# Kernel tuning notes

Hardware: AMD Instinct MI355X
Metric: run time of the kernel (lower is better)

## Reference

```python
import jax, jax.numpy as jnp
import numpy as np


def setup_inputs() -> dict:
    key = jax.random.key(0)
    k1, k2 = jax.random.split(key)
    x = jax.random.normal(k1, (8, 64, 256, 256), dtype=jnp.float32)
    gamma = jax.random.normal(k2, (1,), dtype=jnp.float32)
    return {"x": x, "gamma": gamma}


def reference(x, gamma):
    # NOTE: the torch code does `proj_query -= avg` in-place on a view of x,
    # so proj_value (another view of x) is ALSO mean-centered. We replicate that.
    B, C, H, W = x.shape
    n = H * W
    q = x.reshape(B, C, n)
    q = q - jnp.mean(q, axis=2, keepdims=True)  # centered channels, [B,C,N]
    # energy[b,c,d] = (1/n) * sum_n q[b,c,n]*q[b,d,n]  -> [B,C,C] covariance
    energy = jnp.einsum('bcn,bdn->bcd', q, q) / n
    attention = jax.nn.softmax(energy, axis=-1)
    out = jnp.einsum('bcd,bdn->bcn', attention, q).reshape(B, C, H, W)
    return gamma * out
```

## Files before the change

### kernel.cpp

```cpp
#include <hip/hip_runtime.h>
#include <hip/hip_bf16.h>

typedef __attribute__((ext_vector_type(8))) short short8;
typedef __attribute__((ext_vector_type(4))) short short4v;
typedef __attribute__((ext_vector_type(4))) float f32x4;
typedef __attribute__((ext_vector_type(8))) __bf16 bf16x8;

#define BB 8
#define CC 64
#define NN 65536
#define SPLIT1 64
#define COLS1 (NN / SPLIT1)
#define TILE_C 128
#define NT1 (COLS1 / TILE_C)
#define SPLIT3 128

__device__ inline short f2bf(float f) {
    __hip_bfloat16 h = __float2bfloat16(f);
    return __builtin_bit_cast(short, h);
}

template <typename V>
__device__ inline auto mfma_bf16_impl(V a, V b, f32x4 c, int)
    -> decltype(__builtin_amdgcn_mfma_f32_16x16x32_bf16(a, b, c, 0, 0, 0)) {
    return __builtin_amdgcn_mfma_f32_16x16x32_bf16(a, b, c, 0, 0, 0);
}
template <typename V>
__device__ inline f32x4 mfma_bf16_impl(V a, V b, f32x4 c, long) {
    bf16x8 a2 = __builtin_bit_cast(bf16x8, a);
    bf16x8 b2 = __builtin_bit_cast(bf16x8, b);
    return __builtin_amdgcn_mfma_f32_16x16x32_bf16(a2, b2, c, 0, 0, 0);
}
__device__ inline f32x4 mfma16(short8 a, short8 b, f32x4 c) {
    return mfma_bf16_impl(a, b, c, 0);
}

__device__ inline void stage_tile(const float* __restrict__ xb, int colbase,
                                  float* buf, int tid) {
    const int half = tid >> 5;
    const int sl   = tid & 31;
#pragma unroll
    for (int i = 0; i < 8; ++i) {
        const int row   = i * 8 + half;
        const int gbyte = (sl * 16) ^ ((row & 31) << 4);
        const float* gp = xb + (size_t)row * NN + colbase + (gbyte >> 2);
        float* lp = buf + i * 1024 + tid * 4;
#if __has_builtin(__builtin_amdgcn_global_load_lds)
        __builtin_amdgcn_global_load_lds(
            (const __attribute__((address_space(1))) void*)gp,
            (__attribute__((address_space(3))) void*)lp, 16, 0, 0);
#else
        *reinterpret_cast<f32x4*>(lp) = *reinterpret_cast<const f32x4*>(gp);
#endif
    }
}

__device__ inline void lds_read8(const float* buf, int row, int c0, float* v) {
    const char* rb = (const char*)(buf + row * TILE_C);
    const int swz = (row & 31) << 4;
    const f32x4 u0 = *reinterpret_cast<const f32x4*>(rb + ((c0 * 4) ^ swz));
    const f32x4 u1 = *reinterpret_cast<const f32x4*>(rb + (((c0 * 4) + 16) ^ swz));
    v[0] = u0[0]; v[1] = u0[1]; v[2] = u0[2]; v[3] = u0[3];
    v[4] = u1[0]; v[5] = u1[1]; v[6] = u1[2]; v[7] = u1[3];
}

__device__ inline short8 cvt8(const float* v) {
    short8 r;
#pragma unroll
    for (int j = 0; j < 8; ++j) r[j] = f2bf(v[j]);
    return r;
}

__global__ __launch_bounds__(256) void k1_gram(const float* __restrict__ x,
                                               float* __restrict__ partialG,
                                               float* __restrict__ partialS) {
    __shared__ float lbuf[2][CC * TILE_C];
    const int blk  = blockIdx.x;
    const int b    = blk / SPLIT1;
    const int s    = blk % SPLIT1;
    const int tid  = threadIdx.x;
    const int w    = tid >> 6, lane = tid & 63, lg = lane >> 4, lr = lane & 15;
    const float* xb = x + (size_t)b * CC * NN;
    const int colbase0 = s * COLS1;

    f32x4 acc[4];
#pragma unroll
    for (int dt = 0; dt < 4; ++dt) acc[dt] = (f32x4){0.f, 0.f, 0.f, 0.f};
    float asum = 0.f;

    stage_tile(xb, colbase0, lbuf[0], tid);
    __syncthreads();

    for (int t = 0; t < NT1; ++t) {
        if (t + 1 < NT1)
            stage_tile(xb, colbase0 + (t + 1) * TILE_C, lbuf[(t + 1) & 1], tid);
        const float* buf = lbuf[t & 1];
#pragma unroll
        for (int kk = 0; kk < TILE_C / 32; ++kk) {
            const int c0 = kk * 32 + lg * 8;
            float av[8];
            lds_read8(buf, w * 16 + lr, c0, av);
#pragma unroll
            for (int j = 0; j < 8; ++j) asum += av[j];
            const short8 af = cvt8(av);
#pragma unroll
            for (int dt = 0; dt < 4; ++dt) {
                float bv[8];
                lds_read8(buf, dt * 16 + lr, c0, bv);
                const short8 bf = cvt8(bv);
                acc[dt] = mfma16(af, bf, acc[dt]);
            }
        }
        __syncthreads();
    }
#pragma unroll
    for (int dt = 0; dt < 4; ++dt) {
#pragma unroll
        for (int r = 0; r < 4; ++r) {
            const int c = w * 16 + lg * 4 + r;
            const int d = dt * 16 + lr;
            partialG[(size_t)blk * 4096 + c * 64 + d] = acc[dt][r];
        }
    }
    float v = asum;
    v += __shfl_xor(v, 16);
    v += __shfl_xor(v, 32);
    if (lg == 0) partialS[blk * CC + w * 16 + lr] = v;
}

__global__ __launch_bounds__(256) void k2a_reduceG(const float* __restrict__ partialG,
                                                   float* __restrict__ Gsum) {
    const int gid = blockIdx.x * 256 + threadIdx.x;
    const int b = gid >> 12;
    const int e = gid & 4095;
    float s = 0.f;
    for (int sp = 0; sp < SPLIT1; ++sp)
        s += partialG[(((size_t)(b * SPLIT1 + sp)) << 12) + e];
    Gsum[gid] = s;
}

__global__ __launch_bounds__(256) void k2b_softmax(const float* __restrict__ partialS,
                                                   const float* __restrict__ Gsum,
                                                   unsigned short* __restrict__ att,
                                                   float* __restrict__ offs) {
    __shared__ float mu[CC];
    __shared__ float ener[CC * CC];
    const int b = blockIdx.x;
    const int tid = threadIdx.x;
    if (tid < CC) {
        float s = 0.f;
        for (int sp = 0; sp < SPLIT1; ++sp) s += partialS[(b * SPLIT1 + sp) * CC + tid];
        mu[tid] = s * (1.f / NN);
    }
    __syncthreads();
    const float inv_n = 1.f / NN;
#pragma unroll
    for (int k = 0; k < 16; ++k) {
        const int e = tid + k * 256;
        const int c = e >> 6, d = e & 63;
        ener[e] = Gsum[(b << 12) + e] * inv_n - mu[c] * mu[d];
    }
    __syncthreads();
    const int w = tid >> 6, lane = tid & 63;
    for (int i = 0; i < 16; ++i) {
        const int c = w * 16 + i;
        const float v = ener[c * 64 + lane];
        float m = v;
        for (int off = 32; off > 0; off >>= 1) m = fmaxf(m, __shfl_xor(m, off));
        const float ev = __expf(v - m);
        float sum = ev;
        for (int off = 32; off > 0; off >>= 1) sum += __shfl_xor(sum, off);
        const float a = ev / sum;
        att[(b << 12) + c * 64 + lane] = (unsigned short)f2bf(a);
        float o = a * mu[lane];
        for (int off = 32; off > 0; off >>= 1) o += __shfl_xor(o, off);
        if (lane == 0) offs[b * CC + c] = o;
    }
}

__global__ __launch_bounds__(256) void k3_apply(const float* __restrict__ x,
                                                const unsigned short* __restrict__ att,
                                                const float* __restrict__ offs,
                                                const float* __restrict__ gamma,
                                                float* __restrict__ out) {
    const int blk  = blockIdx.x;
    const int b    = blk / SPLIT3;
    const int s    = blk % SPLIT3;
    const int tid  = threadIdx.x;
    const int w    = tid >> 6, lane = tid & 63, lg = lane >> 4, lr = lane & 15;
    const float g  = gamma[0];

    short8 afr[4][2];
#pragma unroll
    for (int ct = 0; ct < 4; ++ct)
#pragma unroll
        for (int ks = 0; ks < 2; ++ks)
            afr[ct][ks] = *reinterpret_cast<const short8*>(
                att + (((size_t)b) << 12) + (ct * 16 + lr) * 64 + ks * 32 + lg * 8);

    float offv[4][4];
#pragma unroll
    for (int ct = 0; ct < 4; ++ct)
#pragma unroll
        for (int r = 0; r < 4; ++r)
            offv[ct][r] = offs[b * CC + ct * 16 + lg * 4 + r];

    const int colblock = s * (NN / SPLIT3);
    const int GROUPS = (NN / SPLIT3) / (4 * 64);
    for (int itg = 0; itg < GROUPS; ++itg) {
        const int n0 = colblock + (w * GROUPS + itg) * 64;
        f32x4 acc[4][4];
#pragma unroll
        for (int ph = 0; ph < 4; ++ph)
#pragma unroll
            for (int ct = 0; ct < 4; ++ct) acc[ph][ct] = (f32x4){0.f, 0.f, 0.f, 0.f};

#pragma unroll
        for (int ks = 0; ks < 2; ++ks) {
            short8 bfr[4];
            const int d0 = ks * 32 + lg * 8;
            const float* xp = x + ((size_t)(b * CC + d0)) * NN + n0 + lr * 4;
#pragma unroll
            for (int j = 0; j < 8; ++j) {
                const float4 v = *reinterpret_cast<const float4*>(xp + (size_t)j * NN);
                bfr[0][j] = f2bf(v.x);
                bfr[1][j] = f2bf(v.y);
                bfr[2][j] = f2bf(v.z);
                bfr[3][j] = f2bf(v.w);
            }
#pragma unroll
            for (int ct = 0; ct < 4; ++ct) {
#pragma unroll
                for (int ph = 0; ph < 4; ++ph)
                    acc[ph][ct] = mfma16(afr[ct][ks], bfr[ph], acc[ph][ct]);
            }
        }
#pragma unroll
        for (int ct = 0; ct < 4; ++ct) {
#pragma unroll
            for (int r = 0; r < 4; ++r) {
                const int c = ct * 16 + lg * 4 + r;
                const float o = offv[ct][r];
                f32x4 vs;
                vs[0] = g * (acc[0][ct][r] - o);
                vs[1] = g * (acc[1][ct][r] - o);
                vs[2] = g * (acc[2][ct][r] - o);
                vs[3] = g * (acc[3][ct][r] - o);
                __builtin_nontemporal_store(
                    vs, reinterpret_cast<f32x4*>(out + ((size_t)(b * CC + c)) * NN + n0 + lr * 4));
            }
        }
    }
}

extern "C" void kernel_launch(void* const* d_in, const int* in_sizes, int n_in,
                              void* d_out, int out_size, void* d_ws, size_t ws_size,
                              hipStream_t stream) {
    const float* x     = (const float*)d_in[0];
    const float* gamma = (const float*)d_in[1];
    float* out = (float*)d_out;

    float* partialG = out;
    float* partialS = out + (size_t)BB * SPLIT1 * 4096;
    float* Gsum     = partialS + BB * SPLIT1 * CC;
    float* offs     = (float*)d_ws;
    unsigned short* att = (unsigned short*)((char*)d_ws + 4096);

    k1_gram<<<BB * SPLIT1, 256, 0, stream>>>(x, partialG, partialS);
    k2a_reduceG<<<(BB * 4096) / 256, 256, 0, stream>>>(partialG, Gsum);
    k2b_softmax<<<BB, 256, 0, stream>>>(partialS, Gsum, att, offs);
    k3_apply<<<BB * SPLIT3, 256, 0, stream>>>(x, att, offs, gamma, out);
}
```

Measured before the change: 84.24 us.

## Cache bf16 copy of x in workspace during gram pass for apply kernel

The gram kernel now also writes a bf16 copy of each staged x tile to workspace, and the apply kernel reads that half-width copy instead of re-reading and converting fp32 x. This aims to halve the input read bandwidth of the apply pass. In exchange the gram pass gains 64 MiB of extra global writes, so total DRAM traffic is roughly unchanged. The path is only used when the workspace is large enough.

```diff
diff --git a/kernel.cpp b/kernel.cpp
--- a/kernel.cpp
+++ b/kernel.cpp
@@ -45,13 +45,9 @@
         const int gbyte = (sl * 16) ^ ((row & 31) << 4);
         const float* gp = xb + (size_t)row * NN + colbase + (gbyte >> 2);
         float* lp = buf + i * 1024 + tid * 4;
-#if __has_builtin(__builtin_amdgcn_global_load_lds)
         __builtin_amdgcn_global_load_lds(
             (const __attribute__((address_space(1))) void*)gp,
             (__attribute__((address_space(3))) void*)lp, 16, 0, 0);
-#else
-        *reinterpret_cast<f32x4*>(lp) = *reinterpret_cast<const f32x4*>(gp);
-#endif
     }
 }
 
@@ -71,9 +67,11 @@
     return r;
 }
 
+template <bool CACHE>
 __global__ __launch_bounds__(256) void k1_gram(const float* __restrict__ x,
                                                float* __restrict__ partialG,
-                                               float* __restrict__ partialS) {
+                                               float* __restrict__ partialS,
+                                               unsigned short* __restrict__ xbf) {
     __shared__ float lbuf[2][CC * TILE_C];
     const int blk  = blockIdx.x;
     const int b    = blk / SPLIT1;
@@ -81,6 +79,7 @@
     const int tid  = threadIdx.x;
     const int w    = tid >> 6, lane = tid & 63, lg = lane >> 4, lr = lane & 15;
     const float* xb = x + (size_t)b * CC * NN;
+    unsigned short* xbfb = xbf + (size_t)b * CC * NN;
     const int colbase0 = s * COLS1;
 
     f32x4 acc[4];
@@ -94,6 +93,7 @@
     for (int t = 0; t < NT1; ++t) {
         if (t + 1 < NT1)
             stage_tile(xb, colbase0 + (t + 1) * TILE_C, lbuf[(t + 1) & 1], tid);
+        const int colbase = colbase0 + t * TILE_C;
         const float* buf = lbuf[t & 1];
 #pragma unroll
         for (int kk = 0; kk < TILE_C / 32; ++kk) {
@@ -109,6 +109,19 @@
                 lds_read8(buf, dt * 16 + lr, c0, bv);
                 const short8 bf = cvt8(bv);
                 acc[dt] = mfma16(af, bf, acc[dt]);
+            }
+        }
+        if (CACHE) {
+            const int half = tid >> 5, sl = tid & 31;
+#pragma unroll
+            for (int i = 0; i < 8; ++i) {
+                const int row   = i * 8 + half;
+                const int gbyte = (sl * 16) ^ ((row & 31) << 4);
+                const f32x4 v = *reinterpret_cast<const f32x4*>(buf + i * 1024 + tid * 4);
+                short4v sv;
+                sv.x = f2bf(v[0]); sv.y = f2bf(v[1]); sv.z = f2bf(v[2]); sv.w = f2bf(v[3]);
+                *reinterpret_cast<short4v*>(
+                    (char*)(xbfb + (size_t)row * NN + colbase) + (gbyte >> 1)) = sv;
             }
         }
         __syncthreads();
@@ -178,7 +191,9 @@
     }
 }
 
+template <bool CACHE>
 __global__ __launch_bounds__(256) void k3_apply(const float* __restrict__ x,
+                                                const unsigned short* __restrict__ xbf,
                                                 const unsigned short* __restrict__ att,
                                                 const float* __restrict__ offs,
                                                 const float* __restrict__ gamma,
@@ -219,14 +234,23 @@
         for (int ks = 0; ks < 2; ++ks) {
             short8 bfr[4];
             const int d0 = ks * 32 + lg * 8;
-            const float* xp = x + ((size_t)(b * CC + d0)) * NN + n0 + lr * 4;
-#pragma unroll
-            for (int j = 0; j < 8; ++j) {
-                const float4 v = *reinterpret_cast<const float4*>(xp + (size_t)j * NN);
-                bfr[0][j] = f2bf(v.x);
-                bfr[1][j] = f2bf(v.y);
-                bfr[2][j] = f2bf(v.z);
-                bfr[3][j] = f2bf(v.w);
+            if (CACHE) {
+                const unsigned short* xp = xbf + ((size_t)(b * CC + d0)) * NN + n0 + lr * 4;
+#pragma unroll
+                for (int j = 0; j < 8; ++j) {
+                    const short4v v = *reinterpret_cast<const short4v*>(xp + (size_t)j * NN);
+                    bfr[0][j] = v.x; bfr[1][j] = v.y; bfr[2][j] = v.z; bfr[3][j] = v.w;
+                }
+            } else {
+                const float* xp = x + ((size_t)(b * CC + d0)) * NN + n0 + lr * 4;
+#pragma unroll
+                for (int j = 0; j < 8; ++j) {
+                    const float4 v = *reinterpret_cast<const float4*>(xp + (size_t)j * NN);
+                    bfr[0][j] = f2bf(v.x);
+                    bfr[1][j] = f2bf(v.y);
+                    bfr[2][j] = f2bf(v.z);
+                    bfr[3][j] = f2bf(v.w);
+                }
             }
 #pragma unroll
             for (int ct = 0; ct < 4; ++ct) {
@@ -265,9 +289,20 @@
     float* Gsum     = partialS + BB * SPLIT1 * CC;
     float* offs     = (float*)d_ws;
     unsigned short* att = (unsigned short*)((char*)d_ws + 4096);
-
-    k1_gram<<<BB * SPLIT1, 256, 0, stream>>>(x, partialG, partialS);
-    k2a_reduceG<<<(BB * 4096) / 256, 256, 0, stream>>>(partialG, Gsum);
-    k2b_softmax<<<BB, 256, 0, stream>>>(partialS, Gsum, att, offs);
-    k3_apply<<<BB * SPLIT3, 256, 0, stream>>>(x, att, offs, gamma, out);
-}
+    unsigned short* xbf = (unsigned short*)((char*)d_ws + (1 << 20));
+
+    const size_t need = (size_t)(1 << 20) + (size_t)BB * CC * NN * 2;
+    const bool cache = ws_size >= need;
+
+    if (cache) {
+        k1_gram<true><<<BB * SPLIT1, 256, 0, stream>>>(x, partialG, partialS, xbf);
+        k2a_reduceG<<<(BB * 4096) / 256, 256, 0, stream>>>(partialG, Gsum);
+        k2b_softmax<<<BB, 256, 0, stream>>>(partialS, Gsum, att, offs);
+        k3_apply<true><<<BB * SPLIT3, 256, 0, stream>>>(x, xbf, att, offs, gamma, out);
+    } else {
+        k1_gram<false><<<BB * SPLIT1, 256, 0, stream>>>(x, partialG, partialS, xbf);
+        k2a_reduceG<<<(BB * 4096) / 256, 256, 0, stream>>>(partialG, Gsum);
+        k2b_softmax<<<BB, 256, 0, stream>>>(partialS, Gsum, att, offs);
+        k3_apply<false><<<BB * SPLIT3, 256, 0, stream>>>(x, xbf, att, offs, gamma, out);
+    }
+}
```

New measurement: 87.71 us. 4.1% more time.

## Deepen Gram-kernel prefetch to 4-stage ring with explicit vmcnt waits

Applied to the files above, without the earlier changes.

Halves the column tile width and replaces the double-buffered LDS staging with a four-buffer ring that keeps three tiles of global->LDS loads in flight. Each iteration waits with explicit s_waitcnt vmcnt counts plus a single barrier instead of a trailing __syncthreads. The swizzle is adapted to the narrower 16-slot rows, and the diagonal block reuses the already-converted A fragment instead of re-reading LDS. This aims to hide HBM latency better in the memory-bound Gram pass, at the cost of relying on hand-counted outstanding loads, which could break if the compiler reorders memory ops.

```diff
diff --git a/kernel.cpp b/kernel.cpp
--- a/kernel.cpp
+++ b/kernel.cpp
@@ -11,7 +11,7 @@
 #define NN 65536
 #define SPLIT1 64
 #define COLS1 (NN / SPLIT1)
-#define TILE_C 128
+#define TILE_C 64
 #define NT1 (COLS1 / TILE_C)
 #define SPLIT3 128
 
@@ -37,27 +37,23 @@
 
 __device__ inline void stage_tile(const float* __restrict__ xb, int colbase,
                                   float* buf, int tid) {
-    const int half = tid >> 5;
-    const int sl   = tid & 31;
-#pragma unroll
-    for (int i = 0; i < 8; ++i) {
-        const int row   = i * 8 + half;
-        const int gbyte = (sl * 16) ^ ((row & 31) << 4);
+    const int slot  = tid & 15;
+    const int rg    = tid >> 4;
+    const int gbyte = (slot ^ rg) << 4;
+#pragma unroll
+    for (int i = 0; i < 4; ++i) {
+        const int row = i * 16 + rg;
         const float* gp = xb + (size_t)row * NN + colbase + (gbyte >> 2);
         float* lp = buf + i * 1024 + tid * 4;
-#if __has_builtin(__builtin_amdgcn_global_load_lds)
         __builtin_amdgcn_global_load_lds(
             (const __attribute__((address_space(1))) void*)gp,
             (__attribute__((address_space(3))) void*)lp, 16, 0, 0);
-#else
-        *reinterpret_cast<f32x4*>(lp) = *reinterpret_cast<const f32x4*>(gp);
-#endif
     }
 }
 
 __device__ inline void lds_read8(const float* buf, int row, int c0, float* v) {
     const char* rb = (const char*)(buf + row * TILE_C);
-    const int swz = (row & 31) << 4;
+    const int swz = (row & 15) << 4;
     const f32x4 u0 = *reinterpret_cast<const f32x4*>(rb + ((c0 * 4) ^ swz));
     const f32x4 u1 = *reinterpret_cast<const f32x4*>(rb + (((c0 * 4) + 16) ^ swz));
     v[0] = u0[0]; v[1] = u0[1]; v[2] = u0[2]; v[3] = u0[3];
@@ -74,7 +70,7 @@
 __global__ __launch_bounds__(256) void k1_gram(const float* __restrict__ x,
                                                float* __restrict__ partialG,
                                                float* __restrict__ partialS) {
-    __shared__ float lbuf[2][CC * TILE_C];
+    __shared__ float lbuf[4][CC * TILE_C];
     const int blk  = blockIdx.x;
     const int b    = blk / SPLIT1;
     const int s    = blk % SPLIT1;
@@ -88,13 +84,23 @@
     for (int dt = 0; dt < 4; ++dt) acc[dt] = (f32x4){0.f, 0.f, 0.f, 0.f};
     float asum = 0.f;
 
-    stage_tile(xb, colbase0, lbuf[0], tid);
-    __syncthreads();
+    stage_tile(xb, colbase0 + 0 * TILE_C, lbuf[0], tid);
+    stage_tile(xb, colbase0 + 1 * TILE_C, lbuf[1], tid);
+    stage_tile(xb, colbase0 + 2 * TILE_C, lbuf[2], tid);
 
     for (int t = 0; t < NT1; ++t) {
-        if (t + 1 < NT1)
-            stage_tile(xb, colbase0 + (t + 1) * TILE_C, lbuf[(t + 1) & 1], tid);
-        const float* buf = lbuf[t & 1];
+        if (t + 2 < NT1) {
+            asm volatile("s_waitcnt vmcnt(8) lgkmcnt(0)" ::: "memory");
+        } else if (t + 1 < NT1) {
+            asm volatile("s_waitcnt vmcnt(4) lgkmcnt(0)" ::: "memory");
+        } else {
+            asm volatile("s_waitcnt vmcnt(0) lgkmcnt(0)" ::: "memory");
+        }
+        __builtin_amdgcn_s_barrier();
+        if (t + 3 < NT1)
+            stage_tile(xb, colbase0 + (t + 3) * TILE_C, lbuf[(t + 3) & 3], tid);
+
+        const float* buf = lbuf[t & 3];
 #pragma unroll
         for (int kk = 0; kk < TILE_C / 32; ++kk) {
             const int c0 = kk * 32 + lg * 8;
@@ -105,13 +111,17 @@
             const short8 af = cvt8(av);
 #pragma unroll
             for (int dt = 0; dt < 4; ++dt) {
-                float bv[8];
-                lds_read8(buf, dt * 16 + lr, c0, bv);
-                const short8 bf = cvt8(bv);
+                short8 bf;
+                if (dt == w) {
+                    bf = af;
+                } else {
+                    float bv[8];
+                    lds_read8(buf, dt * 16 + lr, c0, bv);
+                    bf = cvt8(bv);
+                }
                 acc[dt] = mfma16(af, bf, acc[dt]);
             }
         }
-        __syncthreads();
     }
 #pragma unroll
     for (int dt = 0; dt < 4; ++dt) {
```

Result: slower. 86.50 us (+2.7%).

## Replace LDS-staged Gram tiles with direct global loads and double split

Applied to the files above, without the earlier changes.

The Gram kernel no longer double-buffers swizzled tiles into shared memory via global_load_lds. Each wave now loads its MFMA operands straight from global memory, and a wave reuses its own A fragment when it is also a B operand. The column split per batch doubles to give more blocks. This removes LDS traffic and barriers, but each block now reads the same rows several times through the caches, with less explicit latency hiding.

```diff
diff --git a/kernel.cpp b/kernel.cpp
--- a/kernel.cpp
+++ b/kernel.cpp
@@ -9,10 +9,8 @@
 #define BB 8
 #define CC 64
 #define NN 65536
-#define SPLIT1 64
+#define SPLIT1 128
 #define COLS1 (NN / SPLIT1)
-#define TILE_C 128
-#define NT1 (COLS1 / TILE_C)
 #define SPLIT3 128
 
 __device__ inline short f2bf(float f) {
@@ -35,31 +33,9 @@
     return mfma_bf16_impl(a, b, c, 0);
 }
 
-__device__ inline void stage_tile(const float* __restrict__ xb, int colbase,
-                                  float* buf, int tid) {
-    const int half = tid >> 5;
-    const int sl   = tid & 31;
-#pragma unroll
-    for (int i = 0; i < 8; ++i) {
-        const int row   = i * 8 + half;
-        const int gbyte = (sl * 16) ^ ((row & 31) << 4);
-        const float* gp = xb + (size_t)row * NN + colbase + (gbyte >> 2);
-        float* lp = buf + i * 1024 + tid * 4;
-#if __has_builtin(__builtin_amdgcn_global_load_lds)
-        __builtin_amdgcn_global_load_lds(
-            (const __attribute__((address_space(1))) void*)gp,
-            (__attribute__((address_space(3))) void*)lp, 16, 0, 0);
-#else
-        *reinterpret_cast<f32x4*>(lp) = *reinterpret_cast<const f32x4*>(gp);
-#endif
-    }
-}
-
-__device__ inline void lds_read8(const float* buf, int row, int c0, float* v) {
-    const char* rb = (const char*)(buf + row * TILE_C);
-    const int swz = (row & 31) << 4;
-    const f32x4 u0 = *reinterpret_cast<const f32x4*>(rb + ((c0 * 4) ^ swz));
-    const f32x4 u1 = *reinterpret_cast<const f32x4*>(rb + (((c0 * 4) + 16) ^ swz));
+__device__ inline void gload8(const float* p, float* v) {
+    const f32x4 u0 = *reinterpret_cast<const f32x4*>(p);
+    const f32x4 u1 = *reinterpret_cast<const f32x4*>(p + 4);
     v[0] = u0[0]; v[1] = u0[1]; v[2] = u0[2]; v[3] = u0[3];
     v[4] = u1[0]; v[5] = u1[1]; v[6] = u1[2]; v[7] = u1[3];
 }
@@ -74,44 +50,43 @@
 __global__ __launch_bounds__(256) void k1_gram(const float* __restrict__ x,
                                                float* __restrict__ partialG,
                                                float* __restrict__ partialS) {
-    __shared__ float lbuf[2][CC * TILE_C];
     const int blk  = blockIdx.x;
     const int b    = blk / SPLIT1;
     const int s    = blk % SPLIT1;
     const int tid  = threadIdx.x;
     const int w    = tid >> 6, lane = tid & 63, lg = lane >> 4, lr = lane & 15;
     const float* xb = x + (size_t)b * CC * NN;
-    const int colbase0 = s * COLS1;
+    const int col0 = s * COLS1;
+
+    const float* rowp0 = xb + (size_t)(0 * 16 + lr) * NN + col0;
+    const float* rowp1 = xb + (size_t)(1 * 16 + lr) * NN + col0;
+    const float* rowp2 = xb + (size_t)(2 * 16 + lr) * NN + col0;
+    const float* rowp3 = xb + (size_t)(3 * 16 + lr) * NN + col0;
+    const float* rowA  = xb + (size_t)(w * 16 + lr) * NN + col0;
 
     f32x4 acc[4];
 #pragma unroll
     for (int dt = 0; dt < 4; ++dt) acc[dt] = (f32x4){0.f, 0.f, 0.f, 0.f};
     float asum = 0.f;
 
-    stage_tile(xb, colbase0, lbuf[0], tid);
-    __syncthreads();
-
-    for (int t = 0; t < NT1; ++t) {
-        if (t + 1 < NT1)
-            stage_tile(xb, colbase0 + (t + 1) * TILE_C, lbuf[(t + 1) & 1], tid);
-        const float* buf = lbuf[t & 1];
-#pragma unroll
-        for (int kk = 0; kk < TILE_C / 32; ++kk) {
-            const int c0 = kk * 32 + lg * 8;
-            float av[8];
-            lds_read8(buf, w * 16 + lr, c0, av);
-#pragma unroll
-            for (int j = 0; j < 8; ++j) asum += av[j];
-            const short8 af = cvt8(av);
-#pragma unroll
-            for (int dt = 0; dt < 4; ++dt) {
-                float bv[8];
-                lds_read8(buf, dt * 16 + lr, c0, bv);
-                const short8 bf = cvt8(bv);
-                acc[dt] = mfma16(af, bf, acc[dt]);
-            }
-        }
-        __syncthreads();
+    for (int c0 = lg * 8; c0 < COLS1; c0 += 32) {
+        float av[8], bv0[8], bv1[8], bv2[8], bv3[8];
+        gload8(rowA + c0, av);
+        if (w != 0) gload8(rowp0 + c0, bv0);
+        if (w != 1) gload8(rowp1 + c0, bv1);
+        if (w != 2) gload8(rowp2 + c0, bv2);
+        if (w != 3) gload8(rowp3 + c0, bv3);
+#pragma unroll
+        for (int j = 0; j < 8; ++j) asum += av[j];
+        const short8 af = cvt8(av);
+        const short8 bf0 = (w == 0) ? af : cvt8(bv0);
+        const short8 bf1 = (w == 1) ? af : cvt8(bv1);
+        const short8 bf2 = (w == 2) ? af : cvt8(bv2);
+        const short8 bf3 = (w == 3) ? af : cvt8(bv3);
+        acc[0] = mfma16(af, bf0, acc[0]);
+        acc[1] = mfma16(af, bf1, acc[1]);
+        acc[2] = mfma16(af, bf2, acc[2]);
+        acc[3] = mfma16(af, bf3, acc[3]);
     }
 #pragma unroll
     for (int dt = 0; dt < 4; ++dt) {
```

Measured after the change: 126.5 us. 1.5x slower.
